# Kernel tuning notes

Hardware: AMD Instinct MI355X
Metric: run time of the kernel (lower is better)

## Reference

```python
import jax, jax.numpy as jnp
import numpy as np

B, N, NIN = 8, 1024, 64
CTX = 3            # context window -> concat dim = NIN*CTX = 192
H = 128            # hidden layer size
NOUT = 2


def _shift_down(x, d):
    # torch: z[:, d:, :] = x[:, :-d, :]
    return jnp.pad(x[:, :-d, :], ((0, 0), (d, 0), (0, 0)))


def _shift_up(x, d):
    # torch: z[:, :-d, :] = x[:, d:, :]
    return jnp.pad(x[:, d:, :], ((0, 0), (0, d), (0, 0)))


def setup_inputs() -> dict:
    key = jax.random.key(0)
    ks = jax.random.split(key, 8)
    n = NIN * CTX  # 192
    s1 = 1.0 / np.sqrt(n)
    s2 = 1.0 / np.sqrt(H)
    return {
        "x_l": jax.random.normal(ks[0], (B, N, NIN), dtype=jnp.float32),
        "W_l": jax.random.uniform(ks[1], (H, n), jnp.float32, -s1, s1),
        "b_l": jax.random.uniform(ks[2], (H,), jnp.float32, -s1, s1),
        "W_r": jax.random.uniform(ks[3], (H, n), jnp.float32, -s1, s1),
        "b_r": jax.random.uniform(ks[4], (H,), jnp.float32, -s1, s1),
        "W_bil": jax.random.uniform(ks[5], (NOUT, H, H), jnp.float32, -s2, s2),
        "b_bil": jax.random.uniform(ks[6], (NOUT,), jnp.float32, -s2, s2),
    }


def reference(x_l, W_l, b_l, W_r, b_r, W_bil, b_bil):
    x_r = x_l  # forward called with x_r=None
    # context expansion (context=3 -> d=1 only): order matches torch append order
    z_l = [x_l]
    z_r = [x_r]
    for d in range(1, CTX // 2 + 1):
        z_l.append(_shift_down(x_l, d)); z_r.append(_shift_up(x_r, d))
        z_l.append(_shift_up(x_l, d));   z_r.append(_shift_down(x_r, d))
    xl = jnp.concatenate(z_l, axis=2)  # [B,N,NIN*CTX]
    xr = jnp.concatenate(z_r, axis=2)
    # MLP (single hidden layer, relu; dropout_rate=0 -> identity)
    hl = jax.nn.relu(jnp.einsum('bnf,hf->bnh', xl, W_l) + b_l)  # [B,N,H]
    hr = jax.nn.relu(jnp.einsum('bnf,hf->bnh', xr, W_r) + b_r)  # [B,N,H]
    # bilinear pairwise score without materializing the expanded [B*N*N,H] tensors
    t = jnp.einsum('bih,khg->bikg', hl, W_bil)                  # [B,N,NOUT,H]
    out = jnp.einsum('bikg,bjg->bijk', t, hr) + b_bil           # [B,N,N,NOUT]
    return out
```

## Files before the change

kernel.cpp:

```cpp
#include <hip/hip_runtime.h>
#include <hip/hip_bf16.h>

typedef __attribute__((ext_vector_type(8))) __bf16 bf16x8;
typedef __attribute__((ext_vector_type(4))) float f32x4;
typedef __attribute__((ext_vector_type(2))) float f32x2;

#define DEVI static __device__ __forceinline__

DEVI unsigned short f2bf(float f) {
    union { float f; unsigned int u; } v; v.f = f;
    unsigned int u = v.u;
    u += 0x7FFFu + ((u >> 16) & 1u);
    return (unsigned short)(u >> 16);
}

__global__ void prep_kernel(const float* __restrict__ Wl,
                            const float* __restrict__ Wr,
                            const float* __restrict__ Wb,
                            unsigned short* __restrict__ WcatT,
                            unsigned short* __restrict__ WtT)
{
    int i = blockIdx.x * 256 + threadIdx.x;
    const int TOT = 256*192 + 256*128;
    if (i >= TOT) return;
    if (i < 256*192) {
        int c = i / 192, kk = i % 192;
        float v;
        if (c < 128) {
            int orig = (kk < 64) ? (kk + 64) : ((kk < 128) ? (kk - 64) : kk);
            v = Wl[c*192 + orig];
        } else {
            int orig = (kk < 64) ? (kk + 128) : (kk - 64);
            v = Wr[(c-128)*192 + orig];
        }
        WcatT[i] = f2bf(v);
    } else {
        int j = i - 256*192;
        int c = j >> 7, h = j & 127;
        int k = c >> 7, g = c & 127;
        WtT[j] = f2bf(Wb[(k*128 + h)*128 + g]);
    }
}

__global__ __launch_bounds__(256) void stage1_kernel(
    const float* __restrict__ x,
    const float* __restrict__ bl,
    const float* __restrict__ br,
    const unsigned short* __restrict__ WcatT,
    const unsigned short* __restrict__ WtT,
    unsigned short* __restrict__ t_out,
    unsigned short* __restrict__ hr_out)
{
    __shared__ unsigned short xwin[18*72];
    __shared__ unsigned short Hbuf[16*264];
    __shared__ unsigned short Tbuf[16*264];

    const int tid = threadIdx.x;
    const int blk = blockIdx.x;
    const int b   = blk >> 6;
    const int n0  = (blk & 63) << 4;

    for (int c = tid; c < 18*16; c += 256) {
        int row = c >> 4, ch = c & 15;
        int n = n0 - 1 + row;
        float4 v = make_float4(0.f, 0.f, 0.f, 0.f);
        if (n >= 0 && n < 1024)
            v = ((const float4*)(x + ((size_t)b*1024 + n)*64))[ch];
        unsigned short* d = &xwin[row*72 + ch*4];
        d[0]=f2bf(v.x); d[1]=f2bf(v.y); d[2]=f2bf(v.z); d[3]=f2bf(v.w);
    }
    __syncthreads();

    const int lane = tid & 63, wave = tid >> 6;
    const int q = lane >> 4, m = lane & 15;

    bf16x8 a[6];
    #pragma unroll
    for (int ks = 0; ks < 6; ++ks) {
        int k = ks*32 + q*8;
        a[ks] = *(const bf16x8*)&xwin[(m + (k >> 6))*72 + (k & 63)];
    }

    #pragma unroll
    for (int cs = 0; cs < 4; ++cs) {
        const int c0 = (wave*4 + cs)*16;
        bf16x8 bw[6];
        #pragma unroll
        for (int ks = 0; ks < 6; ++ks)
            bw[ks] = *(const bf16x8*)(WcatT + (size_t)(c0 + m)*192 + ks*32 + q*8);
        f32x4 acc0 = {0.f,0.f,0.f,0.f};
        #pragma unroll
        for (int ks = 0; ks < 6; ++ks)
            acc0 = __builtin_amdgcn_mfma_f32_16x16x32_bf16(a[ks], bw[ks], acc0, 0, 0, 0);
        const int c = c0 + m;
        const float bias = (c < 128) ? bl[c] : br[c - 128];
        #pragma unroll
        for (int r = 0; r < 4; ++r)
            Hbuf[(q*4 + r)*264 + c] = f2bf(fmaxf(acc0[r] + bias, 0.f));
    }
    __syncthreads();

    {
        int row = tid >> 4, ch = tid & 15;
        bf16x8 v = *(const bf16x8*)&Hbuf[row*264 + 128 + ch*8];
        *(bf16x8*)(hr_out + ((size_t)(b*1024 + n0 + row))*128 + ch*8) = v;
    }

    bf16x8 a2[4];
    #pragma unroll
    for (int ks = 0; ks < 4; ++ks)
        a2[ks] = *(const bf16x8*)&Hbuf[m*264 + ks*32 + q*8];

    #pragma unroll
    for (int cs = 0; cs < 4; ++cs) {
        const int c0 = (wave*4 + cs)*16;
        bf16x8 bw[4];
        #pragma unroll
        for (int ks = 0; ks < 4; ++ks)
            bw[ks] = *(const bf16x8*)(WtT + (size_t)(c0 + m)*128 + ks*32 + q*8);
        f32x4 acc0 = {0.f,0.f,0.f,0.f};
        #pragma unroll
        for (int ks = 0; ks < 4; ++ks)
            acc0 = __builtin_amdgcn_mfma_f32_16x16x32_bf16(a2[ks], bw[ks], acc0, 0, 0, 0);
        const int c = c0 + m;
        #pragma unroll
        for (int r = 0; r < 4; ++r)
            Tbuf[(q*4 + r)*264 + c] = f2bf(acc0[r]);
    }
    __syncthreads();

    for (int c = tid; c < 512; c += 256) {
        int row = c >> 5, ch = c & 31;
        bf16x8 v = *(const bf16x8*)&Tbuf[row*264 + ch*8];
        *(bf16x8*)(t_out + ((size_t)(b*1024 + n0 + row))*256 + ch*8) = v;
    }
}

__global__ __launch_bounds__(256) void stage2_kernel(
    const unsigned short* __restrict__ t_in,
    const unsigned short* __restrict__ hr_in,
    const float* __restrict__ bbil,
    float* __restrict__ out)
{
    const int b = blockIdx.z;
    const int tid = threadIdx.x, lane = tid & 63, wave = tid >> 6;
    const int q = lane >> 4, m = lane & 15;
    const int i0 = blockIdx.x*64 + (wave & 1)*32;
    const int j0 = blockIdx.y*128 + (wave >> 1)*64;

    const unsigned short* tb = t_in  + (size_t)b*1024*256;
    const unsigned short* hb = hr_in + (size_t)b*1024*128;

    f32x4 acc[2][2][4];
    #pragma unroll
    for (int ch = 0; ch < 2; ++ch)
        #pragma unroll
        for (int is = 0; is < 2; ++is)
            #pragma unroll
            for (int js = 0; js < 4; ++js)
                acc[ch][is][js] = (f32x4){0.f,0.f,0.f,0.f};

    #pragma unroll
    for (int ks = 0; ks < 4; ++ks) {
        bf16x8 af[2][2], bf[4];
        #pragma unroll
        for (int is = 0; is < 2; ++is) {
            const unsigned short* rp = tb + (size_t)(i0 + is*16 + m)*256 + ks*32 + q*8;
            af[0][is] = *(const bf16x8*)(rp);
            af[1][is] = *(const bf16x8*)(rp + 128);
        }
        #pragma unroll
        for (int js = 0; js < 4; ++js)
            bf[js] = *(const bf16x8*)(hb + (size_t)(j0 + js*16 + m)*128 + ks*32 + q*8);

        #pragma unroll
        for (int ch = 0; ch < 2; ++ch)
            #pragma unroll
            for (int is = 0; is < 2; ++is)
                #pragma unroll
                for (int js = 0; js < 4; ++js)
                    acc[ch][is][js] = __builtin_amdgcn_mfma_f32_16x16x32_bf16(
                        af[ch][is], bf[js], acc[ch][is][js], 0, 0, 0);
    }

    const float bb0 = bbil[0], bb1 = bbil[1];
    #pragma unroll
    for (int is = 0; is < 2; ++is)
        #pragma unroll
        for (int js = 0; js < 4; ++js)
            #pragma unroll
            for (int r = 0; r < 4; ++r) {
                int i = i0 + is*16 + q*4 + r;
                int j = j0 + js*16 + m;
                f32x2 v = { acc[0][is][js][r] + bb0, acc[1][is][js][r] + bb1 };
                __builtin_nontemporal_store(
                    v, (f32x2*)(out + ((size_t)(b*1024 + i)*1024 + j)*2));
            }
}

extern "C" void kernel_launch(void* const* d_in, const int* in_sizes, int n_in,
                              void* d_out, int out_size, void* d_ws, size_t ws_size,
                              hipStream_t stream)
{
    const float* x    = (const float*)d_in[0];
    const float* Wl   = (const float*)d_in[1];
    const float* bl   = (const float*)d_in[2];
    const float* Wr   = (const float*)d_in[3];
    const float* br   = (const float*)d_in[4];
    const float* Wb   = (const float*)d_in[5];
    const float* bbil = (const float*)d_in[6];
    float* out = (float*)d_out;

    unsigned char* ws = (unsigned char*)d_ws;
    unsigned short* t_ws  = (unsigned short*)(ws);
    unsigned short* hr_ws = (unsigned short*)(ws + (4u<<20));
    unsigned short* WcatT = (unsigned short*)(ws + (6u<<20));
    unsigned short* WtT   = (unsigned short*)(ws + (6u<<20) + 98304);

    prep_kernel<<<320, 256, 0, stream>>>(Wl, Wr, Wb, WcatT, WtT);
    stage1_kernel<<<512, 256, 0, stream>>>(x, bl, br, WcatT, WtT, t_ws, hr_ws);
    stage2_kernel<<<dim3(16, 8, 8), 256, 0, stream>>>(t_ws, hr_ws, bbil, out);
}
```

Before: 117.9 us.

## Fuse three kernels into one cooperative persistent kernel with grid syncs

Replaces the prep, stage1 and stage2 launches with a single cooperative kernel of 256 blocks that uses grid-wide syncs between the phases. Stage1 tiles grow to 32 rows per block, and stage2 blocks each loop over four i-tiles so the grid matches the CU count. The aim is to remove launch gaps and inter-kernel tails. In exchange it adds the cost of grid.sync, and stage2 runs on fewer blocks with less latency hiding. If the cooperative launch fails, it falls back to the three original kernels.

```diff
diff --git a/kernel.cpp b/kernel.cpp
--- a/kernel.cpp
+++ b/kernel.cpp
@@ -1,5 +1,8 @@
 #include <hip/hip_runtime.h>
 #include <hip/hip_bf16.h>
+#include <hip/hip_cooperative_groups.h>
+
+namespace cg = cooperative_groups;
 
 typedef __attribute__((ext_vector_type(8))) __bf16 bf16x8;
 typedef __attribute__((ext_vector_type(4))) float f32x4;
@@ -12,6 +15,212 @@
     unsigned int u = v.u;
     u += 0x7FFFu + ((u >> 16) & 1u);
     return (unsigned short)(u >> 16);
+}
+
+
+__global__ __launch_bounds__(256) void fused_kernel(
+    const float* __restrict__ x,
+    const float* __restrict__ Wl,
+    const float* __restrict__ bl,
+    const float* __restrict__ Wr,
+    const float* __restrict__ br,
+    const float* __restrict__ Wb,
+    const float* __restrict__ bbil,
+    float* __restrict__ out,
+    unsigned short* __restrict__ WcatT,
+    unsigned short* __restrict__ WtT,
+    unsigned short* __restrict__ t_ws,
+    unsigned short* __restrict__ hr_ws)
+{
+    cg::grid_group grid = cg::this_grid();
+
+    __shared__ unsigned short xwin[34*72];
+    __shared__ unsigned short Hbuf[32*264];
+    __shared__ unsigned short Tbuf[32*264];
+
+    const int tid = threadIdx.x;
+    const int blk = blockIdx.x;
+
+    const int TOT = 256*192 + 256*128;
+    for (int i = blk*256 + tid; i < TOT; i += 256*256) {
+        if (i < 256*192) {
+            int c = i / 192, kk = i % 192;
+            float v;
+            if (c < 128) {
+                int orig = (kk < 64) ? (kk + 64) : ((kk < 128) ? (kk - 64) : kk);
+                v = Wl[c*192 + orig];
+            } else {
+                int orig = (kk < 64) ? (kk + 128) : (kk - 64);
+                v = Wr[(c-128)*192 + orig];
+            }
+            WcatT[i] = f2bf(v);
+        } else {
+            int j = i - 256*192;
+            int c = j >> 7, h = j & 127;
+            int k = c >> 7, g = c & 127;
+            WtT[j] = f2bf(Wb[(k*128 + h)*128 + g]);
+        }
+    }
+    __threadfence();
+    grid.sync();
+
+    {
+        const int b1 = blk >> 5;
+        const int n0 = (blk & 31) << 5;
+
+        for (int c = tid; c < 34*16; c += 256) {
+            int row = c >> 4, ch = c & 15;
+            int n = n0 - 1 + row;
+            float4 v = make_float4(0.f, 0.f, 0.f, 0.f);
+            if (n >= 0 && n < 1024)
+                v = ((const float4*)(x + ((size_t)b1*1024 + n)*64))[ch];
+            unsigned short* d = &xwin[row*72 + ch*4];
+            d[0]=f2bf(v.x); d[1]=f2bf(v.y); d[2]=f2bf(v.z); d[3]=f2bf(v.w);
+        }
+        __syncthreads();
+
+        const int lane = tid & 63, wave = tid >> 6;
+        const int q = lane >> 4, m = lane & 15;
+
+        bf16x8 a[2][6];
+        #pragma unroll
+        for (int rs = 0; rs < 2; ++rs)
+            #pragma unroll
+            for (int ks = 0; ks < 6; ++ks) {
+                int row = rs*16 + m;
+                int k = ks*32 + q*8;
+                a[rs][ks] = *(const bf16x8*)&xwin[(row + (k >> 6))*72 + (k & 63)];
+            }
+
+        #pragma unroll
+        for (int cs = 0; cs < 4; ++cs) {
+            const int c0 = (wave*4 + cs)*16;
+            bf16x8 bw[6];
+            #pragma unroll
+            for (int ks = 0; ks < 6; ++ks)
+                bw[ks] = *(const bf16x8*)(WcatT + (size_t)(c0 + m)*192 + ks*32 + q*8);
+            f32x4 acc0 = {0.f,0.f,0.f,0.f}, acc1 = {0.f,0.f,0.f,0.f};
+            #pragma unroll
+            for (int ks = 0; ks < 6; ++ks) {
+                acc0 = __builtin_amdgcn_mfma_f32_16x16x32_bf16(a[0][ks], bw[ks], acc0, 0, 0, 0);
+                acc1 = __builtin_amdgcn_mfma_f32_16x16x32_bf16(a[1][ks], bw[ks], acc1, 0, 0, 0);
+            }
+            const int c = c0 + m;
+            const float bias = (c < 128) ? bl[c] : br[c - 128];
+            #pragma unroll
+            for (int r = 0; r < 4; ++r) {
+                Hbuf[(q*4 + r)*264 + c]      = f2bf(fmaxf(acc0[r] + bias, 0.f));
+                Hbuf[(16 + q*4 + r)*264 + c] = f2bf(fmaxf(acc1[r] + bias, 0.f));
+            }
+        }
+        __syncthreads();
+
+        for (int c = tid; c < 512; c += 256) {
+            int row = c >> 4, ch = c & 15;
+            bf16x8 v = *(const bf16x8*)&Hbuf[row*264 + 128 + ch*8];
+            *(bf16x8*)(hr_ws + ((size_t)(b1*1024 + n0 + row))*128 + ch*8) = v;
+        }
+
+        bf16x8 a2[2][4];
+        #pragma unroll
+        for (int rs = 0; rs < 2; ++rs)
+            #pragma unroll
+            for (int ks = 0; ks < 4; ++ks)
+                a2[rs][ks] = *(const bf16x8*)&Hbuf[(rs*16 + m)*264 + ks*32 + q*8];
+
+        #pragma unroll
+        for (int cs = 0; cs < 4; ++cs) {
+            const int c0 = (wave*4 + cs)*16;
+            bf16x8 bw[4];
+            #pragma unroll
+            for (int ks = 0; ks < 4; ++ks)
+                bw[ks] = *(const bf16x8*)(WtT + (size_t)(c0 + m)*128 + ks*32 + q*8);
+            f32x4 acc0 = {0.f,0.f,0.f,0.f}, acc1 = {0.f,0.f,0.f,0.f};
+            #pragma unroll
+            for (int ks = 0; ks < 4; ++ks) {
+                acc0 = __builtin_amdgcn_mfma_f32_16x16x32_bf16(a2[0][ks], bw[ks], acc0, 0, 0, 0);
+                acc1 = __builtin_amdgcn_mfma_f32_16x16x32_bf16(a2[1][ks], bw[ks], acc1, 0, 0, 0);
+            }
+            const int c = c0 + m;
+            #pragma unroll
+            for (int r = 0; r < 4; ++r) {
+                Tbuf[(q*4 + r)*264 + c]      = f2bf(acc0[r]);
+                Tbuf[(16 + q*4 + r)*264 + c] = f2bf(acc1[r]);
+            }
+        }
+        __syncthreads();
+
+        for (int c = tid; c < 1024; c += 256) {
+            int row = c >> 5, ch = c & 31;
+            bf16x8 v = *(const bf16x8*)&Tbuf[row*264 + ch*8];
+            *(bf16x8*)(t_ws + ((size_t)(b1*1024 + n0 + row))*256 + ch*8) = v;
+        }
+    }
+    __threadfence();
+    grid.sync();
+
+    {
+        const int lane = tid & 63, wave = tid >> 6;
+        const int q = lane >> 4, m = lane & 15;
+        const int b2 = blk >> 5;
+        const int r_ = blk & 31;
+        const int j0 = (r_ >> 2)*128 + (wave >> 1)*64;
+        const int ig = r_ & 3;
+
+        const unsigned short* tb = t_ws  + (size_t)b2*1024*256;
+        const unsigned short* hb = hr_ws + (size_t)b2*1024*128;
+        const float bb0 = bbil[0], bb1 = bbil[1];
+
+        #pragma unroll
+        for (int rep = 0; rep < 4; ++rep) {
+            const int i0 = ig*256 + rep*64 + (wave & 1)*32;
+
+            f32x4 acc[2][2][4];
+            #pragma unroll
+            for (int ch = 0; ch < 2; ++ch)
+                #pragma unroll
+                for (int is = 0; is < 2; ++is)
+                    #pragma unroll
+                    for (int js = 0; js < 4; ++js)
+                        acc[ch][is][js] = (f32x4){0.f,0.f,0.f,0.f};
+
+            #pragma unroll
+            for (int ks = 0; ks < 4; ++ks) {
+                bf16x8 af[2][2], bfr[4];
+                #pragma unroll
+                for (int is = 0; is < 2; ++is) {
+                    const unsigned short* rp = tb + (size_t)(i0 + is*16 + m)*256 + ks*32 + q*8;
+                    af[0][is] = *(const bf16x8*)(rp);
+                    af[1][is] = *(const bf16x8*)(rp + 128);
+                }
+                #pragma unroll
+                for (int js = 0; js < 4; ++js)
+                    bfr[js] = *(const bf16x8*)(hb + (size_t)(j0 + js*16 + m)*128 + ks*32 + q*8);
+
+                #pragma unroll
+                for (int ch = 0; ch < 2; ++ch)
+                    #pragma unroll
+                    for (int is = 0; is < 2; ++is)
+                        #pragma unroll
+                        for (int js = 0; js < 4; ++js)
+                            acc[ch][is][js] = __builtin_amdgcn_mfma_f32_16x16x32_bf16(
+                                af[ch][is], bfr[js], acc[ch][is][js], 0, 0, 0);
+            }
+
+            #pragma unroll
+            for (int is = 0; is < 2; ++is)
+                #pragma unroll
+                for (int js = 0; js < 4; ++js)
+                    #pragma unroll
+                    for (int rr = 0; rr < 4; ++rr) {
+                        int i = i0 + is*16 + q*4 + rr;
+                        int j = j0 + js*16 + m;
+                        f32x2 v = { acc[0][is][js][rr] + bb0, acc[1][is][js][rr] + bb1 };
+                        __builtin_nontemporal_store(
+                            v, (f32x2*)(out + ((size_t)(b2*1024 + i)*1024 + j)*2));
+                    }
+        }
+    }
 }
 
 __global__ void prep_kernel(const float* __restrict__ Wl,
@@ -162,7 +371,7 @@
 
     #pragma unroll
     for (int ks = 0; ks < 4; ++ks) {
-        bf16x8 af[2][2], bf[4];
+        bf16x8 af[2][2], bfr[4];
         #pragma unroll
         for (int is = 0; is < 2; ++is) {
             const unsigned short* rp = tb + (size_t)(i0 + is*16 + m)*256 + ks*32 + q*8;
@@ -171,7 +380,7 @@
         }
         #pragma unroll
         for (int js = 0; js < 4; ++js)
-            bf[js] = *(const bf16x8*)(hb + (size_t)(j0 + js*16 + m)*128 + ks*32 + q*8);
+            bfr[js] = *(const bf16x8*)(hb + (size_t)(j0 + js*16 + m)*128 + ks*32 + q*8);
 
         #pragma unroll
         for (int ch = 0; ch < 2; ++ch)
@@ -180,7 +389,7 @@
                 #pragma unroll
                 for (int js = 0; js < 4; ++js)
                     acc[ch][is][js] = __builtin_amdgcn_mfma_f32_16x16x32_bf16(
-                        af[ch][is], bf[js], acc[ch][is][js], 0, 0, 0);
+                        af[ch][is], bfr[js], acc[ch][is][js], 0, 0, 0);
     }
 
     const float bb0 = bbil[0], bb1 = bbil[1];
@@ -217,7 +426,15 @@
     unsigned short* WcatT = (unsigned short*)(ws + (6u<<20));
     unsigned short* WtT   = (unsigned short*)(ws + (6u<<20) + 98304);
 
-    prep_kernel<<<320, 256, 0, stream>>>(Wl, Wr, Wb, WcatT, WtT);
-    stage1_kernel<<<512, 256, 0, stream>>>(x, bl, br, WcatT, WtT, t_ws, hr_ws);
-    stage2_kernel<<<dim3(16, 8, 8), 256, 0, stream>>>(t_ws, hr_ws, bbil, out);
-}
+    void* args[] = { (void*)&x, (void*)&Wl, (void*)&bl, (void*)&Wr, (void*)&br,
+                     (void*)&Wb, (void*)&bbil, (void*)&out,
+                     (void*)&WcatT, (void*)&WtT, (void*)&t_ws, (void*)&hr_ws };
+    hipError_t err = hipLaunchCooperativeKernel((const void*)fused_kernel,
+                                                dim3(256), dim3(256), args, 0, stream);
+    if (err != hipSuccess) {
+        (void)hipGetLastError();
+        prep_kernel<<<320, 256, 0, stream>>>(Wl, Wr, Wb, WcatT, WtT);
+        stage1_kernel<<<512, 256, 0, stream>>>(x, bl, br, WcatT, WtT, t_ws, hr_ws);
+        stage2_kernel<<<dim3(16, 8, 8), 256, 0, stream>>>(t_ws, hr_ws, bbil, out);
+    }
+}
```

Result: slower. 216.8 us (+83.9%).
